# Kernel tuning notes

Measured on AMD Instinct MI355X. Metric: run time of the kernel, lower is better.

Reference implementation:

```python
import jax, jax.numpy as jnp
import numpy as np

B, S, D, H, DFF, L, V = 256, 77, 512, 8, 2048, 12, 49408
HD = D // H
EPS = 1e-5


def setup_inputs() -> dict:
    key = jax.random.key(0)
    ks = jax.random.split(key, 12)
    s = 0.02
    n = lambda k, shape: s * jax.random.normal(k, shape, dtype=jnp.float32)
    return {
        "input_ids": jax.random.randint(ks[0], (B, S), 0, V),
        "attention_mask": jnp.ones((B, S), dtype=jnp.int32),
        "tok_emb": n(ks[1], (V, D)),
        "pos_emb": n(ks[2], (S, D)),
        "ln1_w": jnp.ones((L, D)), "ln1_b": jnp.zeros((L, D)),
        "q_w": n(ks[3], (L, D, D)), "q_b": jnp.zeros((L, D)),
        "k_w": n(ks[4], (L, D, D)), "k_b": jnp.zeros((L, D)),
        "v_w": n(ks[5], (L, D, D)), "v_b": jnp.zeros((L, D)),
        "o_w": n(ks[6], (L, D, D)), "o_b": jnp.zeros((L, D)),
        "ln2_w": jnp.ones((L, D)), "ln2_b": jnp.zeros((L, D)),
        "fc1_w": n(ks[7], (L, DFF, D)), "fc1_b": jnp.zeros((L, DFF)),
        "fc2_w": n(ks[8], (L, D, DFF)), "fc2_b": jnp.zeros((L, D)),
        "lnf_w": jnp.ones((D,)), "lnf_b": jnp.zeros((D,)),
    }


def layer_norm(x, w, b):
    mu = jnp.mean(x, axis=-1, keepdims=True)
    var = jnp.mean(jnp.square(x - mu), axis=-1, keepdims=True)
    return (x - mu) * jax.lax.rsqrt(var + EPS) * w + b


def quick_gelu(x):
    return x * jax.nn.sigmoid(1.702 * x)


def _encoder(x, mask, layer_params):
    scale = HD ** -0.5

    def heads(t):  # [B,S,D] -> [B,H,S,HD]
        return t.reshape(B, S, H, HD).transpose(0, 2, 1, 3)

    def layer(x, p):
        (ln1w, ln1b, qw, qb, kw, kb, vw, vb, ow, ob,
         ln2w, ln2b, f1w, f1b, f2w, f2b) = p
        h = layer_norm(x, ln1w, ln1b)
        q = heads((h @ qw.T + qb) * scale)
        k = heads(h @ kw.T + kb)
        v = heads(h @ vw.T + vb)
        scores = jnp.einsum('bhqd,bhkd->bhqk', q, k) + mask
        probs = jax.nn.softmax(scores, axis=-1)
        a = jnp.einsum('bhqk,bhkd->bhqd', probs, v)
        a = a.transpose(0, 2, 1, 3).reshape(B, S, D) @ ow.T + ob
        x = x + a
        h = layer_norm(x, ln2w, ln2b)
        h = quick_gelu(h @ f1w.T + f1b)
        h = h @ f2w.T + f2b
        return x + h, None

    x, _ = jax.lax.scan(layer, x, layer_params)
    return x


def reference(input_ids, attention_mask, tok_emb, pos_emb,
              ln1_w, ln1_b, q_w, q_b, k_w, k_b, v_w, v_b, o_w, o_b,
              ln2_w, ln2_b, fc1_w, fc1_b, fc2_w, fc2_b, lnf_w, lnf_b):
    x = tok_emb[input_ids] + pos_emb[None]
    neg = jnp.finfo(x.dtype).min
    causal = jnp.triu(jnp.full((S, S), neg, x.dtype), k=1)[None, None]  # [1,1,S,S]
    pad = (1.0 - attention_mask.astype(x.dtype))[:, None, None, :] * neg  # [B,1,1,S]
    mask = causal + pad  # [B,1,S,S]
    layer_params = (ln1_w, ln1_b, q_w, q_b, k_w, k_b, v_w, v_b, o_w, o_b,
                    ln2_w, ln2_b, fc1_w, fc1_b, fc2_w, fc2_b)
    x = _encoder(x, mask, layer_params)
    last_hidden = layer_norm(x, lnf_w, lnf_b)
    # pooled output: eot token = argmax of input_ids (CLIP convention)
    pooled = last_hidden[jnp.arange(B), jnp.argmax(input_ids, axis=-1)]
    return last_hidden, pooled
```

## Files before the change

### kernel.cpp

```cpp
#include <hip/hip_runtime.h>
#include <math.h>

constexpr int BATCH  = 256;
constexpr int SEQ    = 77;
constexpr int DMODEL = 512;
constexpr int NHEAD  = 8;
constexpr int DHEAD  = 64;
constexpr int DFF    = 2048;
constexpr int NLAYER = 12;
constexpr int NTOK   = BATCH * SEQ;
constexpr int NQKV   = 3 * DMODEL;
constexpr float NEGBIG = -3.402823466e38f;

typedef __attribute__((ext_vector_type(8))) short bf16x8;
typedef __attribute__((ext_vector_type(4))) float f32x4;
typedef __attribute__((ext_vector_type(8))) unsigned short u16x8;

typedef __attribute__((address_space(3))) unsigned char lds_u8;
typedef const __attribute__((address_space(1))) unsigned char g_u8;

__device__ __forceinline__ unsigned short f2bf(float f) {
    unsigned u = __float_as_uint(f);
    u = (u + 0x7FFF + ((u >> 16) & 1)) >> 16;
    return (unsigned short)u;
}
__device__ __forceinline__ float bf2f(unsigned short v) {
    return __uint_as_float((unsigned)v << 16);
}

#define VMCNT4 asm volatile("s_waitcnt vmcnt(4)" ::: "memory")
#define LGKM0  asm volatile("s_waitcnt lgkmcnt(0)" ::: "memory")
#define SCHEDB __builtin_amdgcn_sched_barrier(0)
#define BARRIER do { SCHEDB; __builtin_amdgcn_s_barrier(); SCHEDB; } while (0)

__global__ __launch_bounds__(256) void conv_qkv_kernel(
    const float* __restrict__ qw, const float* __restrict__ kw,
    const float* __restrict__ vw, unsigned short* __restrict__ dst)
{
    int i4 = blockIdx.x * 256 + threadIdx.x;
    int e = i4 * 4;
    int l = e / (NQKV * DMODEL);
    int rem = e - l * (NQKV * DMODEL);
    int row = rem >> 9;
    int k   = rem & 511;
    const float* src;
    float scale = 1.0f;
    size_t lbase = (size_t)l * DMODEL * DMODEL;
    if (row < 512)       { src = qw + lbase + (size_t)row * DMODEL + k; scale = 0.125f; }
    else if (row < 1024) { src = kw + lbase + (size_t)(row - 512) * DMODEL + k; }
    else                 { src = vw + lbase + (size_t)(row - 1024) * DMODEL + k; }
    float4 v = *(const float4*)src;
    ushort4 o;
    o.x = f2bf(v.x * scale); o.y = f2bf(v.y * scale);
    o.z = f2bf(v.z * scale); o.w = f2bf(v.w * scale);
    *(ushort4*)&dst[e] = o;
}

__global__ __launch_bounds__(256) void conv_kernel(
    const float* __restrict__ src, unsigned short* __restrict__ dst)
{
    int e = (blockIdx.x * 256 + threadIdx.x) * 4;
    float4 v = *(const float4*)&src[e];
    ushort4 o;
    o.x = f2bf(v.x); o.y = f2bf(v.y); o.z = f2bf(v.z); o.w = f2bf(v.w);
    *(ushort4*)&dst[e] = o;
}

__global__ __launch_bounds__(256) void bias_qkv_kernel(
    const float* __restrict__ qb, const float* __restrict__ kb,
    const float* __restrict__ vb, float* __restrict__ dst)
{
    int e = blockIdx.x * 256 + threadIdx.x;
    int l = e / NQKV;
    int row = e - l * NQKV;
    float v;
    if (row < 512)       v = qb[l * DMODEL + row] * 0.125f;
    else if (row < 1024) v = kb[l * DMODEL + row - 512];
    else                 v = vb[l * DMODEL + row - 1024];
    dst[e] = v;
}

__global__ __launch_bounds__(256) void embed_kernel(
    const int* __restrict__ ids, const float* __restrict__ tok,
    const float* __restrict__ pos, unsigned short* __restrict__ x)
{
    int f = blockIdx.x * 256 + threadIdx.x;
    int total = NTOK * (DMODEL / 4);
    if (f >= total) return;
    int n  = f >> 7;
    int d4 = f & 127;
    int s  = n % SEQ;
    int id = ids[n];
    float4 t = *(const float4*)&tok[(size_t)id * DMODEL + d4 * 4];
    float4 p = *(const float4*)&pos[(size_t)s  * DMODEL + d4 * 4];
    ushort4 o;
    o.x = f2bf(t.x + p.x); o.y = f2bf(t.y + p.y);
    o.z = f2bf(t.z + p.z); o.w = f2bf(t.w + p.w);
    *(ushort4*)&x[(size_t)n * DMODEL + d4 * 4] = o;
}

template <bool BF16OUT>
__global__ __launch_bounds__(256) void ln_kernel(
    const unsigned short* __restrict__ x, const float* __restrict__ w,
    const float* __restrict__ b, void* __restrict__ out, int nrows)
{
    int row = blockIdx.x * 4 + (threadIdx.x >> 6);
    if (row >= nrows) return;
    int ln = threadIdx.x & 63;
    u16x8 xv = *(const u16x8*)(x + (size_t)row * DMODEL + ln * 8);
    float va[8];
#pragma unroll
    for (int j = 0; j < 8; ++j) va[j] = bf2f(xv[j]);
    float sum = 0.f, sq = 0.f;
#pragma unroll
    for (int j = 0; j < 8; ++j) { sum += va[j]; sq = fmaf(va[j], va[j], sq); }
#pragma unroll
    for (int o = 32; o; o >>= 1) { sum += __shfl_xor(sum, o); sq += __shfl_xor(sq, o); }
    float mu  = sum * (1.0f / DMODEL);
    float var = sq * (1.0f / DMODEL) - mu * mu;
    var = fmaxf(var, 0.0f);
    float inv = 1.0f / sqrtf(var + 1e-5f);
    const float* wp = w + ln * 8;
    const float* bp = b + ln * 8;
    float o8[8];
#pragma unroll
    for (int j = 0; j < 8; ++j) o8[j] = (va[j] - mu) * inv * wp[j] + bp[j];
    if (BF16OUT) {
        u16x8 pk;
#pragma unroll
        for (int j = 0; j < 8; ++j) pk[j] = f2bf(o8[j]);
        *(u16x8*)((unsigned short*)out + (size_t)row * DMODEL + ln * 8) = pk;
    } else {
        float* op = (float*)out + (size_t)row * DMODEL + ln * 8;
        *(float4*)op       = make_float4(o8[0], o8[1], o8[2], o8[3]);
        *(float4*)(op + 4) = make_float4(o8[4], o8[5], o8[6], o8[7]);
    }
}

template <int MODE>
__global__ __launch_bounds__(512, 2) void gemm8_bf16(
    const unsigned short* __restrict__ A, const unsigned short* __restrict__ W,
    const float* __restrict__ bias, const unsigned short* __restrict__ R,
    void* __restrict__ Cout, int M, int N, int K, int gx)
{
    __shared__ __align__(16) char lds[135168];
    const int nwg = gridDim.x;
    const int wg  = blockIdx.x;
    const int q8  = nwg >> 3, r8 = nwg & 7;
    const int xcd = wg & 7, pos = wg >> 3;
    const int start = (xcd < r8) ? xcd * (q8 + 1) : r8 * (q8 + 1) + (xcd - r8) * q8;
    const int newid = start + pos;
    const int by = newid / gx;
    const int bx = newid - by * gx;
    const int m0 = by * 256;
    const int n0 = bx * 256;

    const int tid  = threadIdx.x;
    const int wid  = tid >> 6;
    const int lane = tid & 63;
    const int wr   = wid >> 2;
    const int wc   = wid & 3;
    const int lhi  = lane >> 4;
    const int llo  = lane & 15;

    const int srow  = tid >> 3;
    const int cglob = (tid & 7) ^ (srow & 7);
    const unsigned short* Ap = A + (size_t)(m0 + srow) * K + cglob * 8;
    const unsigned short* Wp = W + (size_t)(n0 + srow) * K + cglob * 8;
    const int NT  = K >> 6;
    const int NT2 = K >> 7;

    const int cb0 = ((0 * 4 + lhi) ^ (llo & 7)) * 16;
    const int cb1 = ((1 * 4 + lhi) ^ (llo & 7)) * 16;
    const int rbA0 = (wr * 128 + 0 * 64 + llo) * 128;
    const int rbA1 = (wr * 128 + 1 * 64 + llo) * 128;
    const int rbB0 = (wc * 64 + 0 * 32 + llo) * 128;
    const int rbB1 = (wc * 64 + 1 * 32 + llo) * 128;

    f32x4 acc[8][4];
#pragma unroll
    for (int i = 0; i < 8; ++i)
#pragma unroll
        for (int j = 0; j < 4; ++j) acc[i][j] = (f32x4){0.f, 0.f, 0.f, 0.f};

    bf16x8 am[4][2], bn0[2][2], bn1[2][2];

    auto stA = [&](int b, int h, int kt) {
#pragma unroll
        for (int i = h * 2; i < h * 2 + 2; ++i)
            __builtin_amdgcn_global_load_lds(
                (g_u8*)(Ap + (size_t)i * 64 * K + kt * 64),
                (lds_u8*)(lds + b * 32768 + i * 8192 + wid * 1024), 16, 0, 0);
    };
    auto stB = [&](int b, int h, int kt) {
#pragma unroll
        for (int i = h * 2; i < h * 2 + 2; ++i)
            __builtin_amdgcn_global_load_lds(
                (g_u8*)(Wp + (size_t)i * 64 * K + kt * 64),
                (lds_u8*)(lds + 65536 + b * 32768 + i * 8192 + wid * 1024), 16, 0, 0);
    };
    auto rdA = [&](int b, int mh) {
        int base = b * 32768 + (mh ? rbA1 : rbA0);
#pragma unroll
        for (int fm = 0; fm < 4; ++fm) {
            am[fm][0] = *(const bf16x8*)(lds + base + fm * 2048 + cb0);
            am[fm][1] = *(const bf16x8*)(lds + base + fm * 2048 + cb1);
        }
    };
    auto rdB = [&](int b, int nh, bf16x8 (&bn)[2][2]) {
        int base = 65536 + b * 32768 + (nh ? rbB1 : rbB0);
#pragma unroll
        for (int fn = 0; fn < 2; ++fn) {
            bn[fn][0] = *(const bf16x8*)(lds + base + fn * 2048 + cb0);
            bn[fn][1] = *(const bf16x8*)(lds + base + fn * 2048 + cb1);
        }
    };
    auto mq = [&](int mh, int nh, bf16x8 (&bn)[2][2]) {
        __builtin_amdgcn_s_setprio(1);
#pragma unroll
        for (int fm = 0; fm < 4; ++fm)
#pragma unroll
            for (int fn = 0; fn < 2; ++fn)
#pragma unroll
                for (int ks = 0; ks < 2; ++ks)
                    acc[mh * 4 + fm][nh * 2 + fn] =
                        __builtin_amdgcn_mfma_f32_16x16x32_bf16(
                            am[fm][ks], bn[fn][ks], acc[mh * 4 + fm][nh * 2 + fn], 0, 0, 0);
        __builtin_amdgcn_s_setprio(0);
    };

    stA(0, 0, 0); stA(0, 1, 0);
    stB(0, 0, 0); stB(0, 1, 0);
    stB(1, 0, 1); stB(1, 1, 1);
    VMCNT4;
    BARRIER;

    for (int it = 0; it < NT2; ++it) {
        const int k1 = 2 * it + 1;
        const int k2 = (2 * it + 2 < NT) ? 2 * it + 2 : NT - 1;
        const int k3 = (2 * it + 3 < NT) ? 2 * it + 3 : NT - 1;
        rdA(0, 0); rdB(0, 0, bn0);
        stA(1, 0, k1);
        LGKM0; BARRIER;
        mq(0, 0, bn0);
        rdB(0, 1, bn1);
        stA(1, 1, k1);
        LGKM0; BARRIER;
        mq(0, 1, bn1);
        rdA(0, 1);
        stB(0, 0, k2);
        LGKM0; BARRIER;
        mq(1, 1, bn1);
        stB(0, 1, k2);
        VMCNT4; BARRIER;
        mq(1, 0, bn0);
        rdA(1, 0); rdB(1, 0, bn0);
        stA(0, 0, k2);
        LGKM0; BARRIER;
        mq(0, 0, bn0);
        rdB(1, 1, bn1);
        stA(0, 1, k2);
        LGKM0; BARRIER;
        mq(0, 1, bn1);
        rdA(1, 1);
        stB(1, 0, k3);
        LGKM0; BARRIER;
        mq(1, 1, bn1);
        stB(1, 1, k3);
        VMCNT4; BARRIER;
        mq(1, 0, bn0);
    }

    if (MODE != 3) {
        unsigned short* sb = (unsigned short*)lds;
#pragma unroll
        for (int j = 0; j < 4; ++j) {
            int colL = wc * 64 + j * 16 + llo;
            float bv = bias[n0 + colL];
#pragma unroll
            for (int i = 0; i < 8; ++i) {
                int rowL = wr * 128 + i * 16 + lhi * 4;
#pragma unroll
                for (int r = 0; r < 4; ++r) {
                    float o = acc[i][j][r] + bv;
                    if (MODE == 2) o = o / (1.0f + __expf(-1.702f * o));
                    sb[(rowL + r) * 264 + colL] = f2bf(o);
                }
            }
        }
        __syncthreads();
        const int l5 = lane & 31, lh2 = lane >> 5;
#pragma unroll
        for (int rr = 0; rr < 16; ++rr) {
            int rowL = rr * 16 + wid * 2 + lh2;
            u16x8 v = *(const u16x8*)&sb[rowL * 264 + l5 * 8];
            *(u16x8*)((unsigned short*)Cout + (size_t)(m0 + rowL) * N + n0 + l5 * 8) = v;
        }
    } else {
        float* sf = (float*)lds;
#pragma unroll
        for (int mh = 0; mh < 2; ++mh) {
            if (mh) __syncthreads();
            if (wr == mh) {
#pragma unroll
                for (int j = 0; j < 4; ++j) {
                    int colL = wc * 64 + j * 16 + llo;
                    float bv = bias[n0 + colL];
#pragma unroll
                    for (int i = 0; i < 8; ++i) {
                        int rowL = i * 16 + lhi * 4;
#pragma unroll
                        for (int r = 0; r < 4; ++r)
                            sf[(rowL + r) * 260 + colL] = acc[i][j][r] + bv;
                    }
                }
            }
            __syncthreads();
#pragma unroll
            for (int rr = 0; rr < 16; ++rr) {
                int rowL = rr * 8 + wid;
                size_t gidx = (size_t)(m0 + mh * 128 + rowL) * N + n0 + lane * 4;
                f32x4 v = *(const f32x4*)&sf[rowL * 260 + lane * 4];
                ushort4 rv = *(const ushort4*)&R[gidx];
                ushort4 o;
                o.x = f2bf(v[0] + bf2f(rv.x));
                o.y = f2bf(v[1] + bf2f(rv.y));
                o.z = f2bf(v[2] + bf2f(rv.z));
                o.w = f2bf(v[3] + bf2f(rv.w));
                *(ushort4*)((unsigned short*)Cout + gidx) = o;
            }
        }
    }
}

__global__ __launch_bounds__(256) void attn_mfma_kernel(
    const unsigned short* __restrict__ qkv, const int* __restrict__ amask,
    unsigned short* __restrict__ out)
{
    const int bh = blockIdx.x;
    const int b = bh >> 3;
    const int h = bh & 7;
    __shared__ __align__(16) char smem[68160];
    char* Qs = smem;
    char* Ks = smem + 10240;
    char* Vt = smem;
    char* Pb = smem + 20480;
    float* ss = (float*)(smem + 40960);
    float* padm = (float*)(smem + 67840);
    const int tid  = threadIdx.x;
    const int wid  = tid >> 6;
    const int lane = tid & 63;
    const int llo  = lane & 15;
    const int lhi  = lane >> 4;

    const size_t vbase = ((size_t)(b * SEQ)) * NQKV + 1024 + h * DHEAD;
    bf16x8 vr0, vr1, vr2;
    {
        int c0 = tid, c1 = tid + 256, c2 = tid + 512;
        vr0 = *(const bf16x8*)&qkv[vbase + (size_t)(c0 >> 3) * NQKV + (c0 & 7) * 8];
        vr1 = *(const bf16x8*)&qkv[vbase + (size_t)(c1 >> 3) * NQKV + (c1 & 7) * 8];
        if (c2 < 616)
            vr2 = *(const bf16x8*)&qkv[vbase + (size_t)(c2 >> 3) * NQKV + (c2 & 7) * 8];
    }

    if (tid < 160) {
        int r = tid >> 1, ch = 10 + (tid & 1);
        bf16x8 z;
#pragma unroll
        for (int j = 0; j < 8; ++j) z[j] = 0;
        *(bf16x8*)(Pb + r * 256 + ((ch ^ (r & 7)) * 16)) = z;
    }

    for (int f = tid; f < 640; f += 256) {
        int r = f >> 3, c = f & 7;
        bf16x8 pq, pk;
        if (r < SEQ) {
            size_t g = ((size_t)(b * SEQ + r)) * NQKV + h * DHEAD + c * 8;
            pq = *(const bf16x8*)&qkv[g];
            pk = *(const bf16x8*)&qkv[g + 512];
        } else {
#pragma unroll
            for (int j = 0; j < 8; ++j) { pq[j] = 0; pk[j] = 0; }
        }
        int byte = r * 128 + ((c * 16) ^ ((r & 7) << 4));
        *(bf16x8*)(Qs + byte) = pq;
        *(bf16x8*)(Ks + byte) = pk;
    }
    for (int s = tid; s < SEQ; s += 256)
        padm[s] = (1.0f - (float)amask[b * SEQ + s]) * NEGBIG;
    __syncthreads();

    for (int t = wid; t < 25; t += 4) {
        int rt = t / 5, ct = t % 5;
        int ar = rt * 16 + llo;
        int br = ct * 16 + llo;
        int aswz = (ar & 7) << 4;
        int bswz = (br & 7) << 4;
        bf16x8 a0 = *(const bf16x8*)(Qs + ar * 128 + ((lhi * 16) ^ aswz));
        bf16x8 a1 = *(const bf16x8*)(Qs + ar * 128 + (((lhi + 4) * 16) ^ aswz));
        bf16x8 b0 = *(const bf16x8*)(Ks + br * 128 + ((lhi * 16) ^ bswz));
        bf16x8 b1 = *(const bf16x8*)(Ks + br * 128 + (((lhi + 4) * 16) ^ bswz));
        f32x4 acc = (f32x4){0.f, 0.f, 0.f, 0.f};
        acc = __builtin_amdgcn_mfma_f32_16x16x32_bf16(a0, b0, acc, 0, 0, 0);
        acc = __builtin_amdgcn_mfma_f32_16x16x32_bf16(a1, b1, acc, 0, 0, 0);
        int ki = ct * 16 + llo;
#pragma unroll
        for (int r = 0; r < 4; ++r) {
            int qi = rt * 16 + lhi * 4 + r;
            ss[qi * 84 + ki] = (ki > qi || ki >= SEQ) ? NEGBIG : (acc[r] + padm[ki]);
        }
    }
    __syncthreads();

    {
        auto writeV = [&](int c, bf16x8 v) {
            int s = c >> 3, d8 = (c & 7) * 8;
            int chunk16 = (s >> 3) * 16, within = (s & 7) * 2;
#pragma unroll
            for (int j = 0; j < 8; ++j) {
                int d = d8 + j;
                *(short*)(Vt + d * 256 + (chunk16 ^ ((d & 7) << 4)) + within) = v[j];
            }
        };
        writeV(tid, vr0);
        writeV(tid + 256, vr1);
        if (tid + 512 < 616) writeV(tid + 512, vr2);
    }

    {
        const int g = lane >> 4;
        const int c = lane & 15;
#pragma unroll
        for (int pass = 0; pass < 5; ++pass) {
            int r = pass * 16 + wid * 4 + g;
            float v0 = ss[r * 84 + c];
            float v1 = ss[r * 84 + c + 16];
            float v2 = ss[r * 84 + c + 32];
            float v3 = ss[r * 84 + c + 48];
            float v4 = ss[r * 84 + c + 64];
            float m = fmaxf(fmaxf(fmaxf(v0, v1), fmaxf(v2, v3)), v4);
#pragma unroll
            for (int o = 8; o; o >>= 1) m = fmaxf(m, __shfl_xor(m, o));
            float e0 = __expf(v0 - m), e1 = __expf(v1 - m), e2 = __expf(v2 - m);
            float e3 = __expf(v3 - m), e4 = __expf(v4 - m);
            float tsum = e0 + e1 + e2 + e3 + e4;
#pragma unroll
            for (int o = 8; o; o >>= 1) tsum += __shfl_xor(tsum, o);
            float rinv = 1.0f / tsum;
            int rswz = (r & 7) << 4;
            int rb = r * 256;
            float ev[5] = {e0, e1, e2, e3, e4};
#pragma unroll
            for (int i = 0; i < 5; ++i) {
                int col = c + i * 16;
                *(short*)(Pb + rb + (((col >> 3) * 16) ^ rswz) + (col & 7) * 2) =
                    (short)f2bf(ev[i] * rinv);
            }
        }
    }
    __syncthreads();

    for (int t = wid; t < 20; t += 4) {
        int rt = t >> 2, ct = t & 3;
        int ar = rt * 16 + llo;
        int br = ct * 16 + llo;
        int aswz = (ar & 7) << 4;
        int bswz = (br & 7) << 4;
        f32x4 acc = (f32x4){0.f, 0.f, 0.f, 0.f};
#pragma unroll
        for (int kc = 0; kc < 3; ++kc) {
            bf16x8 af  = *(const bf16x8*)(Pb + ar * 256 + (((kc * 4 + lhi) * 16) ^ aswz));
            bf16x8 bf_ = *(const bf16x8*)(Vt + br * 256 + (((kc * 4 + lhi) * 16) ^ bswz));
            acc = __builtin_amdgcn_mfma_f32_16x16x32_bf16(af, bf_, acc, 0, 0, 0);
        }
        int d = ct * 16 + llo;
#pragma unroll
        for (int r = 0; r < 4; ++r) {
            int qi = rt * 16 + lhi * 4 + r;
            if (qi < SEQ)
                out[((size_t)(b * SEQ + qi)) * DMODEL + h * DHEAD + d] = f2bf(acc[r]);
        }
    }
}

__global__ __launch_bounds__(64) void pool_kernel(
    const int* __restrict__ ids, const float* __restrict__ lh,
    float* __restrict__ pooled)
{
    int b = blockIdx.x;
    int ln = threadIdx.x;
    __shared__ int sidx;
    if (ln == 0) {
        int best = ids[b * SEQ]; int bi = 0;
        for (int s = 1; s < SEQ; ++s) {
            int vv = ids[b * SEQ + s];
            if (vv > best) { best = vv; bi = s; }
        }
        sidx = bi;
    }
    __syncthreads();
    const float* src = lh + ((size_t)(b * SEQ + sidx)) * DMODEL + ln * 8;
    float* dst = pooled + (size_t)b * DMODEL + ln * 8;
    float4 a = *(const float4*)src;
    float4 c = *(const float4*)(src + 4);
    *(float4*)dst       = a;
    *(float4*)(dst + 4) = c;
}

extern "C" void kernel_launch(void* const* d_in, const int* in_sizes, int n_in,
                              void* d_out, int out_size, void* d_ws, size_t ws_size,
                              hipStream_t stream) {
    const int*   ids   = (const int*)d_in[0];
    const int*   amask = (const int*)d_in[1];
    const float* tok   = (const float*)d_in[2];
    const float* pos   = (const float*)d_in[3];
    const float* ln1w  = (const float*)d_in[4];
    const float* ln1b  = (const float*)d_in[5];
    const float* qw    = (const float*)d_in[6];
    const float* qbias = (const float*)d_in[7];
    const float* kw    = (const float*)d_in[8];
    const float* kbias = (const float*)d_in[9];
    const float* vw    = (const float*)d_in[10];
    const float* vbias = (const float*)d_in[11];
    const float* ow    = (const float*)d_in[12];
    const float* obias = (const float*)d_in[13];
    const float* ln2w  = (const float*)d_in[14];
    const float* ln2b  = (const float*)d_in[15];
    const float* f1w   = (const float*)d_in[16];
    const float* f1b   = (const float*)d_in[17];
    const float* f2w   = (const float*)d_in[18];
    const float* f2b   = (const float*)d_in[19];
    const float* lnfw  = (const float*)d_in[20];
    const float* lnfb  = (const float*)d_in[21];

    char* p = (char*)d_ws;
    unsigned short* x = (unsigned short*)p;    p += (size_t)NTOK * DMODEL * 2;
    unsigned short* hbuf = (unsigned short*)p; p += (size_t)NTOK * DMODEL * 2;
    unsigned short* qkvb = (unsigned short*)p; p += (size_t)NTOK * NQKV * 2;
    unsigned short* ao = (unsigned short*)p;   p += (size_t)NTOK * DMODEL * 2;
    unsigned short* ff = (unsigned short*)p;   p += (size_t)NTOK * DFF * 2;
    unsigned short* wqkv = (unsigned short*)p; p += (size_t)NLAYER * NQKV * DMODEL * 2;
    unsigned short* wo   = (unsigned short*)p; p += (size_t)NLAYER * DMODEL * DMODEL * 2;
    unsigned short* wf1  = (unsigned short*)p; p += (size_t)NLAYER * DFF * DMODEL * 2;
    unsigned short* wf2  = (unsigned short*)p; p += (size_t)NLAYER * DMODEL * DFF * 2;
    float* bqkv = (float*)p;                   p += (size_t)NLAYER * NQKV * 4;

    conv_qkv_kernel<<<(NLAYER * NQKV * DMODEL / 4) / 256, 256, 0, stream>>>(qw, kw, vw, wqkv);
    conv_kernel<<<(NLAYER * DMODEL * DMODEL / 4) / 256, 256, 0, stream>>>(ow, wo);
    conv_kernel<<<(NLAYER * DFF * DMODEL / 4) / 256, 256, 0, stream>>>(f1w, wf1);
    conv_kernel<<<(NLAYER * DMODEL * DFF / 4) / 256, 256, 0, stream>>>(f2w, wf2);
    bias_qkv_kernel<<<(NLAYER * NQKV) / 256, 256, 0, stream>>>(qbias, kbias, vbias, bqkv);

    embed_kernel<<<(NTOK * (DMODEL / 4) + 255) / 256, 256, 0, stream>>>(ids, tok, pos, x);

    const int MB = NTOK / 256;
    dim3 gqkv(MB * (NQKV / 256));
    dim3 g512(MB * (DMODEL / 256));
    dim3 g2048(MB * (DFF / 256));

    for (int l = 0; l < NLAYER; ++l) {
        const size_t wD2 = (size_t)l * DMODEL * DMODEL;
        const size_t wDF = (size_t)l * DFF * DMODEL;
        const size_t oD  = (size_t)l * DMODEL;
        const size_t oF  = (size_t)l * DFF;

        ln_kernel<true><<<NTOK / 4, 256, 0, stream>>>(x, ln1w + oD, ln1b + oD, hbuf, NTOK);
        gemm8_bf16<0><<<gqkv, 512, 0, stream>>>(
            hbuf, wqkv + (size_t)l * NQKV * DMODEL, bqkv + (size_t)l * NQKV, nullptr,
            qkvb, NTOK, NQKV, DMODEL, NQKV / 256);
        attn_mfma_kernel<<<BATCH * NHEAD, 256, 0, stream>>>(qkvb, amask, ao);
        gemm8_bf16<3><<<g512, 512, 0, stream>>>(
            ao, wo + wD2, obias + oD, x, x, NTOK, DMODEL, DMODEL, DMODEL / 256);
        ln_kernel<true><<<NTOK / 4, 256, 0, stream>>>(x, ln2w + oD, ln2b + oD, hbuf, NTOK);
        gemm8_bf16<2><<<g2048, 512, 0, stream>>>(
            hbuf, wf1 + wDF, f1b + oF, nullptr, ff, NTOK, DFF, DMODEL, DFF / 256);
        gemm8_bf16<3><<<g512, 512, 0, stream>>>(
            ff, wf2 + wDF, f2b + oD, x, x, NTOK, DMODEL, DFF, DMODEL / 256);
    }

    float* outf = (float*)d_out;
    ln_kernel<false><<<NTOK / 4, 256, 0, stream>>>(x, lnfw, lnfb, outf, NTOK);
    pool_kernel<<<BATCH, 64, 0, stream>>>(ids, outf, outf + (size_t)NTOK * DMODEL);
}
```

Measured before the change: 3.118 ms.

## Add 32-wide K-step GEMM kernel with swizzled LDS for FC1 GELU layer

Adds a dedicated FC1 GEMM kernel that stages 32-element K slices per buffer (64 KB LDS) with XOR-swizzled layout and launch bounds allowing more resident workgroups. Its epilogue writes GELU output through a swizzled LDS staging area in two half-tile passes and stores with 16-byte vector writes. A full vmcnt(0) wait and barrier are also inserted before the existing kernel's epilogue so outstanding async loads finish before LDS is reused. The smaller K step means more barriers per tile but less LDS per block, trading pipeline depth for occupancy.

```diff
diff --git a/kernel.cpp b/kernel.cpp
--- a/kernel.cpp
+++ b/kernel.cpp
@@ -29,6 +29,7 @@
 }
 
 #define VMCNT4 asm volatile("s_waitcnt vmcnt(4)" ::: "memory")
+#define VMCNT0 asm volatile("s_waitcnt vmcnt(0)" ::: "memory")
 #define LGKM0  asm volatile("s_waitcnt lgkmcnt(0)" ::: "memory")
 #define SCHEDB __builtin_amdgcn_sched_barrier(0)
 #define BARRIER do { SCHEDB; __builtin_amdgcn_s_barrier(); SCHEDB; } while (0)
@@ -271,6 +272,8 @@
         mq(1, 0, bn0);
     }
 
+    VMCNT0; BARRIER;
+
     if (MODE != 3) {
         unsigned short* sb = (unsigned short*)lds;
 #pragma unroll
@@ -329,6 +332,161 @@
                 o.w = f2bf(v[3] + bf2f(rv.w));
                 *(ushort4*)((unsigned short*)Cout + gidx) = o;
             }
+        }
+    }
+}
+
+__global__ __launch_bounds__(512, 4) void gemm32_bf16(
+    const unsigned short* __restrict__ A, const unsigned short* __restrict__ W,
+    const float* __restrict__ bias,
+    unsigned short* __restrict__ Cout, int M, int N, int K, int gx)
+{
+    __shared__ __align__(16) char lds[65536];
+    const int nwg = gridDim.x;
+    const int wg  = blockIdx.x;
+    const int q8  = nwg >> 3, r8 = nwg & 7;
+    const int xcd = wg & 7, pos = wg >> 3;
+    const int start = (xcd < r8) ? xcd * (q8 + 1) : r8 * (q8 + 1) + (xcd - r8) * q8;
+    const int newid = start + pos;
+    const int by = newid / gx;
+    const int bx = newid - by * gx;
+    const int m0 = by * 256;
+    const int n0 = bx * 256;
+
+    const int tid  = threadIdx.x;
+    const int wid  = tid >> 6;
+    const int lane = tid & 63;
+    const int wr   = wid >> 2;
+    const int wc   = wid & 3;
+    const int lhi  = lane >> 4;
+    const int llo  = lane & 15;
+
+    const int srow  = tid >> 2;
+    const int cglob = (tid & 3) ^ ((srow >> 2) & 3);
+    const unsigned short* Ap = A + (size_t)(m0 + srow) * K + cglob * 8;
+    const unsigned short* Wp = W + (size_t)(n0 + srow) * K + cglob * 8;
+    const int NT  = K >> 5;
+    const int NT2 = K >> 6;
+
+    f32x4 acc[8][4];
+#pragma unroll
+    for (int i = 0; i < 8; ++i)
+#pragma unroll
+        for (int j = 0; j < 4; ++j) acc[i][j] = (f32x4){0.f, 0.f, 0.f, 0.f};
+
+    bf16x8 am[4], bn0[2], bn1[2];
+
+    auto stA = [&](int b, int kt) {
+#pragma unroll
+        for (int i = 0; i < 2; ++i)
+            __builtin_amdgcn_global_load_lds(
+                (g_u8*)(Ap + (size_t)i * 128 * K + kt * 32),
+                (lds_u8*)(lds + b * 16384 + i * 8192 + wid * 1024), 16, 0, 0);
+    };
+    auto stB = [&](int b, int kt) {
+#pragma unroll
+        for (int i = 0; i < 2; ++i)
+            __builtin_amdgcn_global_load_lds(
+                (g_u8*)(Wp + (size_t)i * 128 * K + kt * 32),
+                (lds_u8*)(lds + 32768 + b * 16384 + i * 8192 + wid * 1024), 16, 0, 0);
+    };
+    auto rdA = [&](int b, int mh) {
+#pragma unroll
+        for (int fm = 0; fm < 4; ++fm) {
+            int r = wr * 128 + mh * 64 + fm * 16 + llo;
+            am[fm] = *(const bf16x8*)(lds + b * 16384 + r * 64 +
+                                      ((lhi ^ ((r >> 2) & 3)) << 4));
+        }
+    };
+    auto rdB = [&](int b, int nh, bf16x8 (&bn)[2]) {
+#pragma unroll
+        for (int fn = 0; fn < 2; ++fn) {
+            int r = wc * 64 + nh * 32 + fn * 16 + llo;
+            bn[fn] = *(const bf16x8*)(lds + 32768 + b * 16384 + r * 64 +
+                                      ((lhi ^ ((r >> 2) & 3)) << 4));
+        }
+    };
+    auto mq = [&](int mh, int nh, bf16x8 (&bn)[2]) {
+        __builtin_amdgcn_s_setprio(1);
+#pragma unroll
+        for (int fm = 0; fm < 4; ++fm)
+#pragma unroll
+            for (int fn = 0; fn < 2; ++fn)
+                acc[mh * 4 + fm][nh * 2 + fn] =
+                    __builtin_amdgcn_mfma_f32_16x16x32_bf16(
+                        am[fm], bn[fn], acc[mh * 4 + fm][nh * 2 + fn], 0, 0, 0);
+        __builtin_amdgcn_s_setprio(0);
+    };
+
+    stA(0, 0); stB(0, 0);
+    stA(1, 1); stB(1, 1);
+    VMCNT4;
+    BARRIER;
+
+    for (int it = 0; it < NT2; ++it) {
+        const int k2 = (2 * it + 2 < NT) ? 2 * it + 2 : NT - 1;
+        const int k3 = (2 * it + 3 < NT) ? 2 * it + 3 : NT - 1;
+        rdA(0, 0); rdB(0, 0, bn0);
+        LGKM0; BARRIER;
+        mq(0, 0, bn0);
+        rdB(0, 1, bn1);
+        LGKM0; BARRIER;
+        mq(0, 1, bn1);
+        rdA(0, 1);
+        stB(0, k2);
+        LGKM0; BARRIER;
+        mq(1, 1, bn1);
+        stA(0, k2);
+        VMCNT4; BARRIER;
+        mq(1, 0, bn0);
+        rdA(1, 0); rdB(1, 0, bn0);
+        LGKM0; BARRIER;
+        mq(0, 0, bn0);
+        rdB(1, 1, bn1);
+        LGKM0; BARRIER;
+        mq(0, 1, bn1);
+        rdA(1, 1);
+        stB(1, k3);
+        LGKM0; BARRIER;
+        mq(1, 1, bn1);
+        stA(1, k3);
+        VMCNT4; BARRIER;
+        mq(1, 0, bn0);
+    }
+
+    VMCNT0; BARRIER;
+
+    unsigned short* sb = (unsigned short*)lds;
+#pragma unroll
+    for (int mh = 0; mh < 2; ++mh) {
+        if (mh) __syncthreads();
+        if (wr == mh) {
+#pragma unroll
+            for (int j = 0; j < 4; ++j) {
+                int colL = wc * 64 + j * 16 + llo;
+                float bv = bias[n0 + colL];
+#pragma unroll
+                for (int i = 0; i < 8; ++i) {
+                    int rowL = i * 16 + lhi * 4;
+#pragma unroll
+                    for (int r = 0; r < 4; ++r) {
+                        float o = acc[i][j][r] + bv;
+                        o = o / (1.0f + __expf(-1.702f * o));
+                        int rw = rowL + r;
+                        int byte = rw * 512 + ((((colL >> 3) ^ (rw & 7)) << 4)) + (colL & 7) * 2;
+                        *(unsigned short*)((char*)sb + byte) = f2bf(o);
+                    }
+                }
+            }
+        }
+        __syncthreads();
+        const int l5 = lane & 31, lh2 = lane >> 5;
+#pragma unroll
+        for (int rr = 0; rr < 8; ++rr) {
+            int rowL = rr * 16 + wid * 2 + lh2;
+            u16x8 v = *(const u16x8*)((char*)sb + rowL * 512 +
+                                      (((l5 ^ (rowL & 7)) << 4)));
+            *(u16x8*)(Cout + (size_t)(m0 + mh * 128 + rowL) * N + n0 + l5 * 8) = v;
         }
     }
 }
@@ -572,8 +730,8 @@
         gemm8_bf16<3><<<g512, 512, 0, stream>>>(
             ao, wo + wD2, obias + oD, x, x, NTOK, DMODEL, DMODEL, DMODEL / 256);
         ln_kernel<true><<<NTOK / 4, 256, 0, stream>>>(x, ln2w + oD, ln2b + oD, hbuf, NTOK);
-        gemm8_bf16<2><<<g2048, 512, 0, stream>>>(
-            hbuf, wf1 + wDF, f1b + oF, nullptr, ff, NTOK, DFF, DMODEL, DFF / 256);
+        gemm32_bf16<<<g2048, 512, 0, stream>>>(
+            hbuf, wf1 + wDF, f1b + oF, ff, NTOK, DFF, DMODEL, DFF / 256);
         gemm8_bf16<3><<<g512, 512, 0, stream>>>(
             ff, wf2 + wDF, f2b + oD, x, x, NTOK, DMODEL, DFF, DMODEL / 256);
     }
```

New measurement: 9.005 ms. +188.8%, slower.
